# Kernel tuning notes

Hardware: AMD Instinct MI355X
Metric: run time of the kernel (lower is better)

The kernel has to match this reference:

```python
import jax, jax.numpy as jnp
import numpy as np

N = 8192
INPUT_DIM = 3000
HIDDEN_DIM = 512
LATENT_DIM = 30
AVG_DEGREE = 32


def setup_inputs() -> dict:
    key = jax.random.key(0)
    k_x, k_g, k_w0, k_v0, k_v1, k_w1 = jax.random.split(key, 6)

    node_features = jax.random.normal(k_x, (N, INPUT_DIM), dtype=jnp.float32)

    # Binary adjacency, avg degree ~AVG_DEGREE, with self-loops so every
    # softmax row has at least one entry (mirrors typical spatial graphs).
    p = AVG_DEGREE / N
    adj = (jax.random.uniform(k_g, (N, N)) < p).astype(jnp.float32)
    idx = jnp.arange(N)
    graph = adj.at[idx, idx].set(1.0)

    def xavier(k, shape):
        fan_in, fan_out = shape
        limit = float(np.sqrt(6.0 / (fan_in + fan_out)))
        return jax.random.uniform(k, shape, jnp.float32, -limit, limit)

    W0 = xavier(k_w0, (INPUT_DIM, HIDDEN_DIM))
    v0 = xavier(k_v0, (HIDDEN_DIM, 1))
    v1 = xavier(k_v1, (HIDDEN_DIM, 1))
    W1 = xavier(k_w1, (HIDDEN_DIM, LATENT_DIM))

    return {"node_features": node_features, "graph": graph,
            "W0": W0, "v0": v0, "v1": v1, "W1": W1}


def _gat_layer(X_in, graph, W, v0, v1):
    # Projection
    X = X_in @ W                                   # [N, D]
    # Rank-1 pairwise scores, masked by adjacency
    f0 = X @ v0                                    # [N, 1]
    f1 = X @ v1                                    # [N, 1]
    E = graph * (f0 + f1.T)                        # [N, N]
    scores = jax.nn.sigmoid(E) - 0.5               # values kept by to_sparse
    mask = graph != 0
    # Masked softmax over dim=1 (torch.sparse.softmax over nnz of each row;
    # rows with no edges stay all-zero after to_dense)
    neg = jnp.finfo(scores.dtype).min
    w = jnp.where(mask, scores, neg)
    m = jnp.max(w, axis=1, keepdims=True)
    e = jnp.where(mask, jnp.exp(w - m), 0.0)
    s = jnp.sum(e, axis=1, keepdims=True)
    alphas = e / jnp.maximum(s, jnp.asarray(1e-30, scores.dtype))
    # Weighted aggregation + ELU
    return jax.nn.elu(alphas @ X)


def reference(node_features, graph, W0, v0, v1, W1):
    Z = _gat_layer(node_features, graph, W0, v0, v1)  # layer 0 (attention)
    Z = Z @ W1                                        # last layer: proj only
    return Z
```

## Files before the change

### kernel.cpp

```cpp
#include <hip/hip_runtime.h>
#include <hip/hip_bf16.h>
#include <stdint.h>

#define NN   8192
#define KDIM 3000
#define DDIM 512
#define LDIM 30

typedef __attribute__((ext_vector_type(8))) short short8;
typedef __attribute__((ext_vector_type(4))) float float4v;

__device__ __forceinline__ unsigned short f2bf(float f) {
    union { float f; unsigned int u; } v; v.f = f;
    unsigned int r = v.u + 0x7FFF + ((v.u >> 16) & 1);
    return (unsigned short)(r >> 16);
}

__global__ __launch_bounds__(256) void k_convertA(
    const float* __restrict__ A, unsigned short* __restrict__ Abf) {
    int tid = blockIdx.x * 256 + threadIdx.x;
    float4 v = ((const float4*)A)[tid];
    union { unsigned short h[4]; uint2 u; } o;
    o.h[0] = f2bf(v.x); o.h[1] = f2bf(v.y); o.h[2] = f2bf(v.z); o.h[3] = f2bf(v.w);
    ((uint2*)Abf)[tid] = o.u;
}

__global__ void k_prepW(const float* __restrict__ W0,
                        unsigned short* __restrict__ W0T) {
    __shared__ float tile[32][33];
    int t = threadIdx.x;
    int tx = t & 31, ty = t >> 5;
    int k0 = blockIdx.x * 32, n0 = blockIdx.y * 32;
    #pragma unroll
    for (int p = 0; p < 4; p++) {
        int k = k0 + ty + p * 8;
        float val = 0.f;
        if (k < KDIM) val = W0[(size_t)k * DDIM + n0 + tx];
        tile[ty + p * 8][tx] = val;
    }
    __syncthreads();
    #pragma unroll
    for (int p = 0; p < 4; p++) {
        int k = k0 + tx;
        int n = n0 + ty + p * 8;
        if (k < KDIM) W0T[(size_t)n * KDIM + k] = f2bf(tile[tx][ty + p * 8]);
    }
}

#define BM 128
#define BN 64
#define BK 32

__global__ __launch_bounds__(256) void k_gemm_bt(
    const unsigned short* __restrict__ A,
    const unsigned short* __restrict__ BT,
    float* __restrict__ X)
{
    __shared__ __align__(16) unsigned short As[BM * BK];
    __shared__ __align__(16) unsigned short Bs[BN * BK];
    int t = threadIdx.x;
    int w = t >> 6, l = t & 63;
    int m0 = blockIdx.x * BM;
    int n0 = blockIdx.y * BN;
    int wm = (w & 1) * 64, wn = (w >> 1) * 32;

    float4v acc[4][2];
    #pragma unroll
    for (int mf = 0; mf < 4; mf++)
        #pragma unroll
        for (int nf = 0; nf < 2; nf++)
            acc[mf][nf] = (float4v){0.f, 0.f, 0.f, 0.f};

    int ar0 = t >> 2;
    int ar1 = ar0 + 64;
    int akk = (t & 3) * 8;
    int br  = t >> 2;

    const int lA = (l & 15);
    const int qA = (l >> 4) * 8;

    for (int k0 = 0; k0 < KDIM; k0 += BK) {
        uint4 av0 = {0, 0, 0, 0}, av1 = {0, 0, 0, 0}, bv = {0, 0, 0, 0};
        bool kok = (k0 + akk) < KDIM;
        if (kok) {
            av0 = *(const uint4*)(A + (size_t)(m0 + ar0) * KDIM + k0 + akk);
            av1 = *(const uint4*)(A + (size_t)(m0 + ar1) * KDIM + k0 + akk);
            bv  = *(const uint4*)(BT + (size_t)(n0 + br) * KDIM + k0 + akk);
        }
        __syncthreads();
        *(uint4*)(As + ar0 * BK + akk) = av0;
        *(uint4*)(As + ar1 * BK + akk) = av1;
        *(uint4*)(Bs + br  * BK + akk) = bv;
        __syncthreads();

        short8 af[4], bfr[2];
        #pragma unroll
        for (int mf = 0; mf < 4; mf++)
            af[mf] = *(const short8*)(As + (wm + mf * 16 + lA) * BK + qA);
        #pragma unroll
        for (int nf = 0; nf < 2; nf++)
            bfr[nf] = *(const short8*)(Bs + (wn + nf * 16 + lA) * BK + qA);
        #pragma unroll
        for (int mf = 0; mf < 4; mf++)
            #pragma unroll
            for (int nf = 0; nf < 2; nf++)
                acc[mf][nf] = __builtin_amdgcn_mfma_f32_16x16x32_bf16(
                    af[mf], bfr[nf], acc[mf][nf], 0, 0, 0);
    }

    int rq = (l >> 4) * 4;
    #pragma unroll
    for (int mf = 0; mf < 4; mf++) {
        #pragma unroll
        for (int nf = 0; nf < 2; nf++) {
            int col = n0 + wn + nf * 16 + (l & 15);
            int row = m0 + wm + mf * 16 + rq;
            #pragma unroll
            for (int r = 0; r < 4; r++)
                X[(size_t)(row + r) * DDIM + col] = acc[mf][nf][r];
        }
    }
}

__global__ __launch_bounds__(256) void k_f01(
    const float* __restrict__ X,
    const float* __restrict__ v0,
    const float* __restrict__ v1,
    float* __restrict__ f0, float* __restrict__ f1)
{
    int w = threadIdx.x >> 6, l = threadIdx.x & 63;
    int i = blockIdx.x * 4 + w;
    const float* xr = X + (size_t)i * DDIM + l * 8;
    float4 xa = *(const float4*)(xr);
    float4 xb = *(const float4*)(xr + 4);
    float4 a0 = *(const float4*)(v0 + l * 8);
    float4 b0 = *(const float4*)(v0 + l * 8 + 4);
    float4 a1 = *(const float4*)(v1 + l * 8);
    float4 b1 = *(const float4*)(v1 + l * 8 + 4);
    float p0 = xa.x*a0.x + xa.y*a0.y + xa.z*a0.z + xa.w*a0.w
             + xb.x*b0.x + xb.y*b0.y + xb.z*b0.z + xb.w*b0.w;
    float p1 = xa.x*a1.x + xa.y*a1.y + xa.z*a1.z + xa.w*a1.w
             + xb.x*b1.x + xb.y*b1.y + xb.z*b1.z + xb.w*b1.w;
    #pragma unroll
    for (int off = 32; off; off >>= 1) {
        p0 += __shfl_down(p0, off);
        p1 += __shfl_down(p1, off);
    }
    if (l == 0) { f0[i] = p0; f1[i] = p1; }
}

#define CAP 1024
__global__ __launch_bounds__(256) void k_aggregate(
    const float* __restrict__ G,
    const float* __restrict__ X,
    const float* __restrict__ f0,
    const float* __restrict__ f1,
    const float* __restrict__ W1,
    float* __restrict__ out)
{
    __shared__ int cnt;
    __shared__ int   jlist[CAP];
    __shared__ float elist[CAP];
    __shared__ float zrow[DDIM];
    __shared__ float red[256];
    int t = threadIdx.x;
    int i = blockIdx.x;
    if (t == 0) cnt = 0;
    __syncthreads();

    float f0i = f0[i];
    const float* grow = G + (size_t)i * NN;
    #pragma unroll
    for (int it = 0; it < 8; it++) {
        int base = (it * 256 + t) * 4;
        float4 gv = *(const float4*)(grow + base);
        float g[4] = {gv.x, gv.y, gv.z, gv.w};
        #pragma unroll
        for (int m = 0; m < 4; m++) {
            if (g[m] != 0.f) {
                int j = base + m;
                float xe = f0i + f1[j];
                float sg = 1.0f / (1.0f + __expf(-xe));
                float e  = __expf(sg - 0.5f);
                int p = atomicAdd(&cnt, 1);
                if (p < CAP) { jlist[p] = j; elist[p] = e; }
            }
        }
    }
    __syncthreads();

    int n = cnt < CAP ? cnt : CAP;
    float s = 0.f;
    for (int k = 0; k < n; k++) s += elist[k];
    float inv = 1.0f / fmaxf(s, 1e-30f);

    float a0 = 0.f, a1 = 0.f;
    for (int k = 0; k < n; k++) {
        int j = jlist[k];
        float e = elist[k];
        float2 xv = *(const float2*)(X + (size_t)j * DDIM + t * 2);
        a0 += e * xv.x;
        a1 += e * xv.y;
    }
    a0 *= inv; a1 *= inv;
    zrow[2 * t]     = a0 > 0.f ? a0 : __expf(a0) - 1.0f;
    zrow[2 * t + 1] = a1 > 0.f ? a1 : __expf(a1) - 1.0f;
    __syncthreads();

    int c = t & 31, slab = t >> 5;
    float p = 0.f;
    if (c < LDIM) {
        #pragma unroll 4
        for (int q = 0; q < 64; q++) {
            int d = slab * 64 + q;
            p += zrow[d] * W1[d * LDIM + c];
        }
    }
    red[t] = p;
    __syncthreads();
    if (t < LDIM) {
        float sum = 0.f;
        #pragma unroll
        for (int s2 = 0; s2 < 8; s2++) sum += red[s2 * 32 + t];
        out[(size_t)i * LDIM + t] = sum;
    }
}

extern "C" void kernel_launch(void* const* d_in, const int* in_sizes, int n_in,
                              void* d_out, int out_size, void* d_ws, size_t ws_size,
                              hipStream_t stream) {
    (void)in_sizes; (void)n_in; (void)out_size; (void)ws_size;
    const float* nf = (const float*)d_in[0];
    const float* G  = (const float*)d_in[1];
    const float* W0 = (const float*)d_in[2];
    const float* v0 = (const float*)d_in[3];
    const float* v1 = (const float*)d_in[4];
    const float* W1 = (const float*)d_in[5];
    float* out = (float*)d_out;

    char* ws = (char*)d_ws;
    unsigned short* Abf = (unsigned short*)(ws);
    unsigned short* W0T = (unsigned short*)(ws + 49152000);
    float* X  = (float*)(ws + 49152000 + 3072000);
    float* f0 = (float*)(ws + 49152000 + 3072000 + 16777216);
    float* f1 = (float*)(ws + 49152000 + 3072000 + 16777216 + 32768);

    hipLaunchKernelGGL(k_convertA, dim3(24000), dim3(256), 0, stream, nf, Abf);
    hipLaunchKernelGGL(k_prepW, dim3(94, 16), dim3(256), 0, stream, W0, W0T);
    hipLaunchKernelGGL(k_gemm_bt, dim3(64, 8), dim3(256), 0, stream, Abf, W0T, X);
    hipLaunchKernelGGL(k_f01, dim3(2048), dim3(256), 0, stream, X, v0, v1, f0, f1);
    hipLaunchKernelGGL(k_aggregate, dim3(8192), dim3(256), 0, stream, G, X, f0, f1, W1, out);
}
```

Measured before the change: 550.1 us.

## Pad K to 3072, use direct global-to-LDS loads, gather bf16 X in aggregation

The conversion and W0 transpose now pad the K dimension to 3072 with zeros, so the GEMM can drop its bounds checks. Tiles are loaded straight into LDS with global_load_lds at 64-wide K steps, which halves the number of barriers per K. The GEMM also writes a bf16 copy of X, and the aggregation gathers neighbour rows from that copy with a 4-way unrolled loop, halving gather bytes. In exchange there are extra X writes and reduced precision in the aggregation.

```diff
diff --git a/kernel.cpp b/kernel.cpp
--- a/kernel.cpp
+++ b/kernel.cpp
@@ -1,28 +1,43 @@
 #include <hip/hip_runtime.h>
-#include <hip/hip_bf16.h>
 #include <stdint.h>
 
 #define NN   8192
 #define KDIM 3000
+#define KP   3072
 #define DDIM 512
 #define LDIM 30
 
 typedef __attribute__((ext_vector_type(8))) short short8;
 typedef __attribute__((ext_vector_type(4))) float float4v;
 
+__device__ __forceinline__ float bf2f(unsigned short h) {
+    union { unsigned int u; float f; } v; v.u = ((unsigned int)h) << 16; return v.f;
+}
 __device__ __forceinline__ unsigned short f2bf(float f) {
     union { float f; unsigned int u; } v; v.f = f;
     unsigned int r = v.u + 0x7FFF + ((v.u >> 16) & 1);
     return (unsigned short)(r >> 16);
 }
-
-__global__ __launch_bounds__(256) void k_convertA(
+__device__ __forceinline__ void gl_lds16(const void* g, void* l) {
+    __builtin_amdgcn_global_load_lds(
+        (const __attribute__((address_space(1))) unsigned int*)g,
+        (__attribute__((address_space(3))) unsigned int*)l, 16, 0, 0);
+}
+
+__global__ __launch_bounds__(384) void k_convertA(
     const float* __restrict__ A, unsigned short* __restrict__ Abf) {
-    int tid = blockIdx.x * 256 + threadIdx.x;
-    float4 v = ((const float4*)A)[tid];
-    union { unsigned short h[4]; uint2 u; } o;
-    o.h[0] = f2bf(v.x); o.h[1] = f2bf(v.y); o.h[2] = f2bf(v.z); o.h[3] = f2bf(v.w);
-    ((uint2*)Abf)[tid] = o.u;
+    int row = blockIdx.x, t = threadIdx.x;
+    int k = t * 8;
+    uint4 o = {0, 0, 0, 0};
+    if (k < KDIM) {
+        const float* src = A + (size_t)row * KDIM + k;
+        float4 a = *(const float4*)src;
+        float4 b = *(const float4*)(src + 4);
+        unsigned short* h = (unsigned short*)&o;
+        h[0] = f2bf(a.x); h[1] = f2bf(a.y); h[2] = f2bf(a.z); h[3] = f2bf(a.w);
+        h[4] = f2bf(b.x); h[5] = f2bf(b.y); h[6] = f2bf(b.z); h[7] = f2bf(b.w);
+    }
+    *(uint4*)(Abf + (size_t)row * KP + k) = o;
 }
 
 __global__ void k_prepW(const float* __restrict__ W0,
@@ -43,25 +58,23 @@
     for (int p = 0; p < 4; p++) {
         int k = k0 + tx;
         int n = n0 + ty + p * 8;
-        if (k < KDIM) W0T[(size_t)n * KDIM + k] = f2bf(tile[tx][ty + p * 8]);
+        W0T[(size_t)n * KP + k] = f2bf(tile[tx][ty + p * 8]);
     }
 }
 
 #define BM 128
 #define BN 64
-#define BK 32
-
-__global__ __launch_bounds__(256) void k_gemm_bt(
+
+__global__ __launch_bounds__(256) void k_gemm(
     const unsigned short* __restrict__ A,
     const unsigned short* __restrict__ BT,
-    float* __restrict__ X)
+    float* __restrict__ X,
+    unsigned short* __restrict__ Xbf)
 {
-    __shared__ __align__(16) unsigned short As[BM * BK];
-    __shared__ __align__(16) unsigned short Bs[BN * BK];
-    int t = threadIdx.x;
-    int w = t >> 6, l = t & 63;
-    int m0 = blockIdx.x * BM;
-    int n0 = blockIdx.y * BN;
+    __shared__ __align__(16) unsigned short As[2][BM][32];
+    __shared__ __align__(16) unsigned short Bs[2][BN][32];
+    int t = threadIdx.x, w = t >> 6, l = t & 63;
+    int m0 = blockIdx.x * BM, n0 = blockIdx.y * BN;
     int wm = (w & 1) * 64, wn = (w >> 1) * 32;
 
     float4v acc[4][2];
@@ -71,41 +84,45 @@
         for (int nf = 0; nf < 2; nf++)
             acc[mf][nf] = (float4v){0.f, 0.f, 0.f, 0.f};
 
-    int ar0 = t >> 2;
-    int ar1 = ar0 + 64;
-    int akk = (t & 3) * 8;
-    int br  = t >> 2;
-
-    const int lA = (l & 15);
+    int lr = l >> 2;
+    int lk = (l & 3) * 8;
+    const unsigned short* Abase = A  + (size_t)m0 * KP;
+    const unsigned short* Bbase = BT + (size_t)n0 * KP;
+    const int lA = l & 15;
     const int qA = (l >> 4) * 8;
 
-    for (int k0 = 0; k0 < KDIM; k0 += BK) {
-        uint4 av0 = {0, 0, 0, 0}, av1 = {0, 0, 0, 0}, bv = {0, 0, 0, 0};
-        bool kok = (k0 + akk) < KDIM;
-        if (kok) {
-            av0 = *(const uint4*)(A + (size_t)(m0 + ar0) * KDIM + k0 + akk);
-            av1 = *(const uint4*)(A + (size_t)(m0 + ar1) * KDIM + k0 + akk);
-            bv  = *(const uint4*)(BT + (size_t)(n0 + br) * KDIM + k0 + akk);
+    for (int k0 = 0; k0 < KP; k0 += 64) {
+        if (k0) __syncthreads();
+        #pragma unroll
+        for (int p = 0; p < 4; p++) {
+            int q = w * 4 + p, h = q >> 3, rb = q & 7;
+            gl_lds16(Abase + (size_t)(rb * 16 + lr) * KP + k0 + h * 32 + lk,
+                     &As[h][rb * 16][0]);
+        }
+        #pragma unroll
+        for (int p = 0; p < 2; p++) {
+            int q = w * 2 + p, h = q >> 2, rb = q & 3;
+            gl_lds16(Bbase + (size_t)(rb * 16 + lr) * KP + k0 + h * 32 + lk,
+                     &Bs[h][rb * 16][0]);
         }
         __syncthreads();
-        *(uint4*)(As + ar0 * BK + akk) = av0;
-        *(uint4*)(As + ar1 * BK + akk) = av1;
-        *(uint4*)(Bs + br  * BK + akk) = bv;
-        __syncthreads();
-
-        short8 af[4], bfr[2];
-        #pragma unroll
-        for (int mf = 0; mf < 4; mf++)
-            af[mf] = *(const short8*)(As + (wm + mf * 16 + lA) * BK + qA);
-        #pragma unroll
-        for (int nf = 0; nf < 2; nf++)
-            bfr[nf] = *(const short8*)(Bs + (wn + nf * 16 + lA) * BK + qA);
-        #pragma unroll
-        for (int mf = 0; mf < 4; mf++)
+
+        #pragma unroll
+        for (int h = 0; h < 2; h++) {
+            short8 af[4], bfr[2];
+            #pragma unroll
+            for (int mf = 0; mf < 4; mf++)
+                af[mf] = *(const short8*)&As[h][wm + mf * 16 + lA][qA];
             #pragma unroll
             for (int nf = 0; nf < 2; nf++)
-                acc[mf][nf] = __builtin_amdgcn_mfma_f32_16x16x32_bf16(
-                    af[mf], bfr[nf], acc[mf][nf], 0, 0, 0);
+                bfr[nf] = *(const short8*)&Bs[h][wn + nf * 16 + lA][qA];
+            #pragma unroll
+            for (int mf = 0; mf < 4; mf++)
+                #pragma unroll
+                for (int nf = 0; nf < 2; nf++)
+                    acc[mf][nf] = __builtin_amdgcn_mfma_f32_16x16x32_bf16(
+                        af[mf], bfr[nf], acc[mf][nf], 0, 0, 0);
+        }
     }
 
     int rq = (l >> 4) * 4;
@@ -113,11 +130,14 @@
     for (int mf = 0; mf < 4; mf++) {
         #pragma unroll
         for (int nf = 0; nf < 2; nf++) {
-            int col = n0 + wn + nf * 16 + (l & 15);
+            int col = n0 + wn + nf * 16 + lA;
             int row = m0 + wm + mf * 16 + rq;
             #pragma unroll
-            for (int r = 0; r < 4; r++)
-                X[(size_t)(row + r) * DDIM + col] = acc[mf][nf][r];
+            for (int r = 0; r < 4; r++) {
+                float v = acc[mf][nf][r];
+                X  [(size_t)(row + r) * DDIM + col] = v;
+                Xbf[(size_t)(row + r) * DDIM + col] = f2bf(v);
+            }
         }
     }
 }
@@ -152,7 +172,7 @@
 #define CAP 1024
 __global__ __launch_bounds__(256) void k_aggregate(
     const float* __restrict__ G,
-    const float* __restrict__ X,
+    const unsigned short* __restrict__ Xbf,
     const float* __restrict__ f0,
     const float* __restrict__ f1,
     const float* __restrict__ W1,
@@ -195,12 +215,29 @@
     float inv = 1.0f / fmaxf(s, 1e-30f);
 
     float a0 = 0.f, a1 = 0.f;
-    for (int k = 0; k < n; k++) {
+    int k = 0;
+    for (; k + 4 <= n; k += 4) {
+        int j0 = jlist[k], j1 = jlist[k+1], j2 = jlist[k+2], j3 = jlist[k+3];
+        float e0 = elist[k], e1 = elist[k+1], e2 = elist[k+2], e3 = elist[k+3];
+        unsigned int x0 = *(const unsigned int*)(Xbf + (size_t)j0 * DDIM + t * 2);
+        unsigned int x1 = *(const unsigned int*)(Xbf + (size_t)j1 * DDIM + t * 2);
+        unsigned int x2 = *(const unsigned int*)(Xbf + (size_t)j2 * DDIM + t * 2);
+        unsigned int x3 = *(const unsigned int*)(Xbf + (size_t)j3 * DDIM + t * 2);
+        a0 += e0 * bf2f((unsigned short)(x0 & 0xFFFFu))
+            + e1 * bf2f((unsigned short)(x1 & 0xFFFFu))
+            + e2 * bf2f((unsigned short)(x2 & 0xFFFFu))
+            + e3 * bf2f((unsigned short)(x3 & 0xFFFFu));
+        a1 += e0 * bf2f((unsigned short)(x0 >> 16))
+            + e1 * bf2f((unsigned short)(x1 >> 16))
+            + e2 * bf2f((unsigned short)(x2 >> 16))
+            + e3 * bf2f((unsigned short)(x3 >> 16));
+    }
+    for (; k < n; k++) {
         int j = jlist[k];
         float e = elist[k];
-        float2 xv = *(const float2*)(X + (size_t)j * DDIM + t * 2);
-        a0 += e * xv.x;
-        a1 += e * xv.y;
+        unsigned int xw = *(const unsigned int*)(Xbf + (size_t)j * DDIM + t * 2);
+        a0 += e * bf2f((unsigned short)(xw & 0xFFFFu));
+        a1 += e * bf2f((unsigned short)(xw >> 16));
     }
     a0 *= inv; a1 *= inv;
     zrow[2 * t]     = a0 > 0.f ? a0 : __expf(a0) - 1.0f;
@@ -240,14 +277,15 @@
 
     char* ws = (char*)d_ws;
     unsigned short* Abf = (unsigned short*)(ws);
-    unsigned short* W0T = (unsigned short*)(ws + 49152000);
-    float* X  = (float*)(ws + 49152000 + 3072000);
-    float* f0 = (float*)(ws + 49152000 + 3072000 + 16777216);
-    float* f1 = (float*)(ws + 49152000 + 3072000 + 16777216 + 32768);
-
-    hipLaunchKernelGGL(k_convertA, dim3(24000), dim3(256), 0, stream, nf, Abf);
-    hipLaunchKernelGGL(k_prepW, dim3(94, 16), dim3(256), 0, stream, W0, W0T);
-    hipLaunchKernelGGL(k_gemm_bt, dim3(64, 8), dim3(256), 0, stream, Abf, W0T, X);
+    unsigned short* W0T = (unsigned short*)(ws + 50331648);
+    float*          X   = (float*)(ws + 50331648 + 3145728);
+    unsigned short* Xbf = (unsigned short*)(ws + 50331648 + 3145728 + 16777216);
+    float* f0 = (float*)(ws + 50331648 + 3145728 + 16777216 + 8388608);
+    float* f1 = (float*)(ws + 50331648 + 3145728 + 16777216 + 8388608 + 32768);
+
+    hipLaunchKernelGGL(k_convertA, dim3(8192), dim3(384), 0, stream, nf, Abf);
+    hipLaunchKernelGGL(k_prepW, dim3(96, 16), dim3(256), 0, stream, W0, W0T);
+    hipLaunchKernelGGL(k_gemm, dim3(64, 8), dim3(256), 0, stream, Abf, W0T, X, Xbf);
     hipLaunchKernelGGL(k_f01, dim3(2048), dim3(256), 0, stream, X, v0, v1, f0, f1);
-    hipLaunchKernelGGL(k_aggregate, dim3(8192), dim3(256), 0, stream, G, X, f0, f1, W1, out);
-}
+    hipLaunchKernelGGL(k_aggregate, dim3(8192), dim3(256), 0, stream, G, Xbf, f0, f1, W1, out);
+}
```

Result: faster. 516.8 us (-6.1%).
